# Kernel optimization log

Measured on AMD Instinct MI355X. Metric: run time of the kernel, lower is better.

The kernel has to match this reference:

```python
import jax, jax.numpy as jnp
import numpy as np

D = 128
N_DATA = 100000
N_TASK = 20000
E = 1000000


def _conv_params(key, d):
    ks = jax.random.split(key, 9)
    s = 1.0 / np.sqrt(d)
    return dict(
        Wmn=jax.random.uniform(ks[0], (d, d), jnp.float32, -s, s),
        bmn=jnp.zeros((d,), jnp.float32),
        Wme=jax.random.uniform(ks[1], (d, 1), jnp.float32, -1.0, 1.0),
        bme=jnp.zeros((d,), jnp.float32),
        Wgn=jax.random.uniform(ks[2], (d, d), jnp.float32, -s, s),
        bgn=jnp.zeros((d,), jnp.float32),
        Wge=jax.random.uniform(ks[3], (d, 1), jnp.float32, -1.0, 1.0),
        bge=jnp.zeros((d,), jnp.float32),
        bias=jnp.zeros((d,), jnp.float32),  # HeteConvLayer bias, zeros-init
    )


def setup_inputs() -> dict:
    key = jax.random.key(0)
    ks = jax.random.split(key, 12)
    inp = {
        'x_data': jax.random.normal(ks[0], (N_DATA, D), jnp.float32),
        'x_task': jax.random.normal(ks[1], (N_TASK, D), jnp.float32),
        'src_dt': jax.random.randint(ks[2], (E,), 0, N_DATA, jnp.int32),
        'dst_dt': jax.random.randint(ks[3], (E,), 0, N_TASK, jnp.int32),
        'ef_dt': jax.random.uniform(ks[4], (E, 1), jnp.float32),
        'src_td': jax.random.randint(ks[5], (E,), 0, N_TASK, jnp.int32),
        'dst_td': jax.random.randint(ks[6], (E,), 0, N_DATA, jnp.int32),
        'ef_td': jax.random.uniform(ks[7], (E, 1), jnp.float32),
    }
    # two separate HeteConvLayers (cfg.kg.hete=True)
    for name, k in (('dt', ks[8]), ('td', ks[9])):
        for pn, pv in _conv_params(k, D).items():
            inp[pn + '_' + name] = pv
    s = 1.0 / np.sqrt(D)
    inp['Ws_data'] = jax.random.uniform(ks[10], (D, D), jnp.float32, -s, s)
    inp['bs_data'] = jnp.zeros((D,), jnp.float32)
    inp['Ws_task'] = jax.random.uniform(ks[11], (D, D), jnp.float32, -s, s)
    inp['bs_task'] = jnp.zeros((D,), jnp.float32)
    return inp


def _hete_conv(x_neigh, src, dst, ef, Wmn, bmn, Wme, bme, Wgn, bgn, Wge, bge, bias, n_out):
    xj = x_neigh[src]                                   # [E, D] gather
    msg = xj @ Wmn.T + bmn + ef @ Wme.T + bme           # [E, D]
    gate = jax.nn.sigmoid(xj @ Wgn.T + bgn + ef @ Wge.T + bge) - 0.5  # gate_bias
    msg = msg * gate
    return jax.ops.segment_sum(msg, dst, num_segments=n_out) + bias


def _self_layer(x, Ws, bs):
    return (jax.nn.sigmoid(x @ Ws.T + bs) + 0.5) * x    # SelfLayer, gate_bias=True


def reference(x_data, x_task, src_dt, dst_dt, ef_dt, src_td, dst_td, ef_td,
              Wmn_dt, bmn_dt, Wme_dt, bme_dt, Wgn_dt, bgn_dt, Wge_dt, bge_dt, bias_dt,
              Wmn_td, bmn_td, Wme_td, bme_td, Wgn_td, bgn_td, Wge_td, bge_td, bias_td,
              Ws_data, bs_data, Ws_task, bs_task):
    # message type (data, property, task): neigh=data, self=task
    agg_task = _hete_conv(x_data, src_dt, dst_dt, ef_dt,
                          Wmn_dt, bmn_dt, Wme_dt, bme_dt,
                          Wgn_dt, bgn_dt, Wge_dt, bge_dt, bias_dt, N_TASK)
    # message type (task, property, data): neigh=task, self=data
    agg_data = _hete_conv(x_task, src_td, dst_td, ef_td,
                          Wmn_td, bmn_td, Wme_td, bme_td,
                          Wgn_td, bgn_td, Wge_td, bge_td, bias_td, N_DATA)
    # add self-transform, aggr='add', then Postlayer = ReLU
    data_emb = jax.nn.relu(agg_data + _self_layer(x_data, Ws_data, bs_data))
    task_emb = jax.nn.relu(agg_task + _self_layer(x_task, Ws_task, bs_task))
    # concatenate node-type outputs along node axis for a single output array
    return jnp.concatenate([data_emb, task_emb], axis=0)
```

## Files before the change

### kernel.cpp

```cpp
#include <hip/hip_runtime.h>
#include <hip/hip_bf16.h>
#include <cstdint>
#include <cstddef>

#define D_DIM 128

typedef __attribute__((ext_vector_type(8))) short short8;
typedef __attribute__((ext_vector_type(4))) float f32x4;

__device__ __forceinline__ float sigmoid_fast(float z) {
  return __builtin_amdgcn_rcpf(1.0f + __expf(-z));
}

__device__ __forceinline__ unsigned short f2bf(float f) {
  union { float f; unsigned u; } v; v.f = f;
  unsigned r = v.u + 0x7FFF + ((v.u >> 16) & 1);
  return (unsigned short)(r >> 16);
}
__device__ __forceinline__ float bf_lo(unsigned u) { return __uint_as_float(u << 16); }
__device__ __forceinline__ float bf_hi(unsigned u) { return __uint_as_float(u & 0xFFFF0000u); }

__global__ __launch_bounds__(256) void wconv_kernel(
    const float* __restrict__ s0, const float* __restrict__ s1, const float* __restrict__ s2,
    const float* __restrict__ s3, const float* __restrict__ s4, const float* __restrict__ s5,
    short* __restrict__ dst) {
  int idx = blockIdx.x * 256 + threadIdx.x;
  int mat = idx >> 12;
  int pos = (idx & 4095) * 4;
  const float* s = (mat == 0) ? s0 : (mat == 1) ? s1 : (mat == 2) ? s2
                 : (mat == 3) ? s3 : (mat == 4) ? s4 : s5;
  float4 f = *(const float4*)(s + pos);
  short4 o;
  o.x = (short)f2bf(f.x); o.y = (short)f2bf(f.y);
  o.z = (short)f2bf(f.z); o.w = (short)f2bf(f.w);
  *(short4*)(dst + mat * 16384 + pos) = o;
}

__global__ __launch_bounds__(256) void node_mfma_kernel(
    const float* __restrict__ x,
    const short* __restrict__ Wmnb, const short* __restrict__ Wgnb, const short* __restrict__ Wsb,
    const float* __restrict__ bmn, const float* __restrict__ bme,
    const float* __restrict__ bgn, const float* __restrict__ bge,
    const float* __restrict__ bs, const float* __restrict__ bias_other,
    unsigned int* __restrict__ YG, float* __restrict__ out_init, int n) {
  __shared__ unsigned sh[32][132];
  const int t = threadIdx.x;
  const int wave = t >> 6, lane = t & 63;
  const int q = lane >> 4, l15 = lane & 15;
  const int ng = wave >> 1;
  const int h = (wave & 1) * 64;
  const int base_node = blockIdx.x * 32;
  const int node_base = base_node + ng * 16;

  short8 a[4];
  {
    int m = node_base + l15;
    int mc = m < n ? m : (n - 1);
    const float* xrow = x + (size_t)mc * D_DIM;
#pragma unroll
    for (int ks = 0; ks < 4; ++ks) {
      float4 f0 = *(const float4*)(xrow + ks * 32 + q * 8);
      float4 f1 = *(const float4*)(xrow + ks * 32 + q * 8 + 4);
      union { short8 s; __hip_bfloat162 hh[4]; } u;
      u.hh[0] = __float22bfloat162_rn({f0.x, f0.y});
      u.hh[1] = __float22bfloat162_rn({f0.z, f0.w});
      u.hh[2] = __float22bfloat162_rn({f1.x, f1.y});
      u.hh[3] = __float22bfloat162_rn({f1.z, f1.w});
      a[ks] = u.s;
    }
  }

  f32x4 accY[4], accG[4], accS[4];
#pragma unroll
  for (int nt = 0; nt < 4; ++nt) { accY[nt] = {0,0,0,0}; accG[nt] = {0,0,0,0}; accS[nt] = {0,0,0,0}; }

#pragma unroll
  for (int nt = 0; nt < 4; ++nt) {
    const int row = h + nt * 16 + l15;
#pragma unroll
    for (int ks = 0; ks < 4; ++ks) {
      const int off = row * D_DIM + ks * 32 + q * 8;
      short8 bm  = *(const short8*)(Wmnb + off);
      short8 bg  = *(const short8*)(Wgnb + off);
      short8 bsw = *(const short8*)(Wsb + off);
      accY[nt] = __builtin_amdgcn_mfma_f32_16x16x32_bf16(a[ks], bm,  accY[nt], 0, 0, 0);
      accG[nt] = __builtin_amdgcn_mfma_f32_16x16x32_bf16(a[ks], bg,  accG[nt], 0, 0, 0);
      accS[nt] = __builtin_amdgcn_mfma_f32_16x16x32_bf16(a[ks], bsw, accS[nt], 0, 0, 0);
    }
  }

#pragma unroll
  for (int nt = 0; nt < 4; ++nt) {
    int d = h + nt * 16 + l15;
    float bmv = bmn[d] + bme[d];
    float bgv = bgn[d] + bge[d];
#pragma unroll
    for (int r = 0; r < 4; ++r) {
      union { __hip_bfloat162 hh; unsigned u; } pck;
      pck.hh = __float22bfloat162_rn({accY[nt][r] + bmv, accG[nt][r] + bgv});
      sh[ng * 16 + q * 4 + r][d] = pck.u;
    }
  }
  __syncthreads();
#pragma unroll
  for (int it = 0; it < 4; ++it) {
    int idx = (it * 256 + t) * 4;
    int nl = idx >> 7, dd = idx & 127;
    int node = base_node + nl;
    if (node < n)
      *(uint4*)(YG + (size_t)node * D_DIM + dd) = *(const uint4*)&sh[nl][dd];
  }
  __syncthreads();

  float* shf = (float*)sh;
#pragma unroll
  for (int nt = 0; nt < 4; ++nt) {
    int d = h + nt * 16 + l15;
    float bsv = bs[d];
#pragma unroll
    for (int r = 0; r < 4; ++r)
      shf[(ng * 16 + q * 4 + r) * 132 + d] = sigmoid_fast(accS[nt][r] + bsv) + 0.5f;
  }
  __syncthreads();
#pragma unroll
  for (int it = 0; it < 4; ++it) {
    int idx = (it * 256 + t) * 4;
    int nl = idx >> 7, dd = idx & 127;
    int node = base_node + nl;
    if (node < n) {
      float4 xv = *(const float4*)(x + (size_t)node * D_DIM + dd);
      float4 bo = *(const float4*)(bias_other + dd);
      const float* sp = &shf[nl * 132 + dd];
      float4 o;
      o.x = sp[0] * xv.x + bo.x;
      o.y = sp[1] * xv.y + bo.y;
      o.z = sp[2] * xv.z + bo.z;
      o.w = sp[3] * xv.w + bo.w;
      *(float4*)(out_init + (size_t)node * D_DIM + dd) = o;
    }
  }
}


__global__ __launch_bounds__(256) void hist0_kernel(
    const int* __restrict__ dst_dt, const int* __restrict__ dst_td,
    int* __restrict__ ghist, int nbt, int NB, int E) {
  __shared__ int lh[768];
  int t = threadIdx.x;
  lh[t] = 0; lh[t + 256] = 0; lh[t + 512] = 0;
  __syncthreads();
  for (int i = blockIdx.x * 256 + t; i < E; i += gridDim.x * 256) {
    atomicAdd(&lh[dst_dt[i] >> 6], 1);
    atomicAdd(&lh[nbt + (dst_td[i] >> 8)], 1);
  }
  __syncthreads();
#pragma unroll
  for (int k = 0; k < 3; ++k) {
    int b = t + k * 256;
    int c = lh[b];
    if (b < NB && c) atomicAdd(&ghist[b], c);
  }
}

__global__ __launch_bounds__(256) void bucket_scan_kernel(
    const int* __restrict__ ghist, int* __restrict__ bbase, int* __restrict__ bcur,
    int* __restrict__ offsets, int NB, int n_tot) {
  __shared__ int sc[256];
  int t = threadIdx.x;
  int i0 = t * 3;
  int c0 = (i0     < NB) ? ghist[i0]     : 0;
  int c1 = (i0 + 1 < NB) ? ghist[i0 + 1] : 0;
  int c2 = (i0 + 2 < NB) ? ghist[i0 + 2] : 0;
  int tot = c0 + c1 + c2;
  sc[t] = tot; __syncthreads();
  for (int s = 1; s < 256; s <<= 1) {
    int u = (t >= s) ? sc[t - s] : 0;
    __syncthreads(); sc[t] += u; __syncthreads();
  }
  int base = sc[t] - tot;
  if (i0     < NB) { bbase[i0]     = base;           bcur[i0]     = base; }
  if (i0 + 1 < NB) { bbase[i0 + 1] = base + c0;      bcur[i0 + 1] = base + c0; }
  if (i0 + 2 < NB) { bbase[i0 + 2] = base + c0 + c1; bcur[i0 + 2] = base + c0 + c1; }
  if (t == 255) { bbase[NB] = sc[255]; offsets[n_tot] = sc[255]; }
}

__global__ __launch_bounds__(256) void sort_a_kernel(
    const int* __restrict__ src_dt, const int* __restrict__ dst_dt, const float* __restrict__ ef_dt,
    const int* __restrict__ src_td, const int* __restrict__ dst_td, const float* __restrict__ ef_td,
    int* __restrict__ bcur, int2* __restrict__ eA, int nbt, int NB, int E) {
  __shared__ int lh[768];
  __shared__ int lcur[768];
  int t = threadIdx.x;
  lh[t] = 0; lh[t + 256] = 0; lh[t + 512] = 0;
  __syncthreads();
  int e0 = blockIdx.x * 4096;
  int e1 = min(E, e0 + 4096);
  for (int i = e0 + t; i < e1; i += 256) {
    atomicAdd(&lh[dst_dt[i] >> 6], 1);
    atomicAdd(&lh[nbt + (dst_td[i] >> 8)], 1);
  }
  __syncthreads();
#pragma unroll
  for (int k = 0; k < 3; ++k) {
    int b = t + k * 256;
    int c = lh[b];
    if (b < NB && c) lcur[b] = atomicAdd(&bcur[b], c);
  }
  __syncthreads();
  for (int i = e0 + t; i < e1; i += 256) {
    int c = dst_dt[i];
    int bkt = c >> 6;
    int pos = atomicAdd(&lcur[bkt], 1);
    eA[pos] = make_int2(src_dt[i],
        (int)((__float_as_uint(ef_dt[i]) & 0xFFFFFF00u) | (unsigned)(c & 63)));
    int cd = dst_td[i];
    int bkt2 = nbt + (cd >> 8);
    int pos2 = atomicAdd(&lcur[bkt2], 1);
    eA[pos2] = make_int2(src_td[i],
        (int)((__float_as_uint(ef_td[i]) & 0xFFFFFF00u) | (unsigned)(cd & 255)));
  }
}

__global__ __launch_bounds__(256) void sort_b_kernel(
    const int2* __restrict__ eA, const int* __restrict__ bbase,
    int* __restrict__ offsets, int2* __restrict__ eB,
    int nbt, int n_task, int n_tot) {
  __shared__ int lh[256], sc[256], lcur[256];
  int b = blockIdx.x, t = threadIdx.x;
  int base = bbase[b];
  int cnt = bbase[b + 1] - base;
  int c0, nloc;
  if (b < nbt) { c0 = b << 6; nloc = min(64, n_task - c0); }
  else { c0 = n_task + ((b - nbt) << 8); nloc = min(256, n_tot - c0); }
  lh[t] = 0; __syncthreads();
  for (int i = base + t; i < base + cnt; i += 256)
    atomicAdd(&lh[((unsigned)eA[i].y) & 255u], 1);
  __syncthreads();
  int v = lh[t];
  sc[t] = v; __syncthreads();
  for (int s = 1; s < 256; s <<= 1) {
    int u = (t >= s) ? sc[t - s] : 0;
    __syncthreads(); sc[t] += u; __syncthreads();
  }
  int ex = sc[t] - v;
  lcur[t] = base + ex;
  if (t < nloc) offsets[c0 + t] = base + ex;
  __syncthreads();
  for (int i = base + t; i < base + cnt; i += 256) {
    int2 e = eA[i];
    int pos = atomicAdd(&lcur[((unsigned)e.y) & 255u], 1);
    eB[pos] = e;
  }
}

__device__ __forceinline__ void gstep(float2& acc, int2 e, const unsigned* __restrict__ YG,
                                      int lane, float2 wme, float2 wge) {
  uint2 yg = *(const uint2*)(YG + (size_t)e.x * D_DIM + 2 * lane);
  float f = __int_as_float(e.y & (int)0xFFFFFF00);
  float g0 = sigmoid_fast(fmaf(f, wge.x, bf_hi(yg.x))) - 0.5f;
  float g1 = sigmoid_fast(fmaf(f, wge.y, bf_hi(yg.y))) - 0.5f;
  acc.x += fmaf(f, wme.x, bf_lo(yg.x)) * g0;
  acc.y += fmaf(f, wme.y, bf_lo(yg.y)) * g1;
}

__global__ __launch_bounds__(256) void gather_kernel(
    const unsigned* __restrict__ YG_dt, const unsigned* __restrict__ YG_td,
    const int* __restrict__ offsets, const int2* __restrict__ edata,
    const float* __restrict__ Wme_dt, const float* __restrict__ Wge_dt,
    const float* __restrict__ Wme_td, const float* __restrict__ Wge_td,
    float* __restrict__ out, int n_task, int n_data) {
  int w = (int)((blockIdx.x * 256u + threadIdx.x) >> 6);
  int lane = threadIdx.x & 63;
  if (w >= n_task + n_data) return;
  bool is_dt = w < n_task;
  const unsigned* YG = is_dt ? YG_dt : YG_td;
  const float* Wme = is_dt ? Wme_dt : Wme_td;
  const float* Wge = is_dt ? Wge_dt : Wge_td;
  size_t orow = is_dt ? (size_t)(n_data + w) : (size_t)(w - n_task);
  int beg = __builtin_amdgcn_readfirstlane(offsets[w]);
  int end = __builtin_amdgcn_readfirstlane(offsets[w + 1]);
  float2 wme = *(const float2*)(Wme + 2 * lane);
  float2 wge = *(const float2*)(Wge + 2 * lane);
  float* op = out + orow * D_DIM + 2 * lane;
  float2 acc0 = *(const float2*)op;
  float2 acc1 = {0.0f, 0.0f};
  int p = beg;
  for (; p + 8 <= end; p += 8) {
    int2 e0 = edata[p],     e1 = edata[p + 1], e2 = edata[p + 2], e3 = edata[p + 3];
    int2 e4 = edata[p + 4], e5 = edata[p + 5], e6 = edata[p + 6], e7 = edata[p + 7];
    gstep(acc0, e0, YG, lane, wme, wge);
    gstep(acc1, e1, YG, lane, wme, wge);
    gstep(acc0, e2, YG, lane, wme, wge);
    gstep(acc1, e3, YG, lane, wme, wge);
    gstep(acc0, e4, YG, lane, wme, wge);
    gstep(acc1, e5, YG, lane, wme, wge);
    gstep(acc0, e6, YG, lane, wme, wge);
    gstep(acc1, e7, YG, lane, wme, wge);
  }
  for (; p + 2 <= end; p += 2) {
    int2 e0 = edata[p], e1 = edata[p + 1];
    gstep(acc0, e0, YG, lane, wme, wge);
    gstep(acc1, e1, YG, lane, wme, wge);
  }
  if (p < end) gstep(acc0, edata[p], YG, lane, wme, wge);
  acc0.x = fmaxf(acc0.x + acc1.x, 0.0f);
  acc0.y = fmaxf(acc0.y + acc1.y, 0.0f);
  *(float2*)op = acc0;
}

extern "C" void kernel_launch(void* const* d_in, const int* in_sizes, int n_in,
                              void* d_out, int out_size, void* d_ws, size_t ws_size,
                              hipStream_t stream) {
  const float* x_data  = (const float*)d_in[0];
  const float* x_task  = (const float*)d_in[1];
  const int*   src_dt  = (const int*)d_in[2];
  const int*   dst_dt  = (const int*)d_in[3];
  const float* ef_dt   = (const float*)d_in[4];
  const int*   src_td  = (const int*)d_in[5];
  const int*   dst_td  = (const int*)d_in[6];
  const float* ef_td   = (const float*)d_in[7];
  const float* Wmn_dt  = (const float*)d_in[8];
  const float* bmn_dt  = (const float*)d_in[9];
  const float* Wme_dt  = (const float*)d_in[10];
  const float* bme_dt  = (const float*)d_in[11];
  const float* Wgn_dt  = (const float*)d_in[12];
  const float* bgn_dt  = (const float*)d_in[13];
  const float* Wge_dt  = (const float*)d_in[14];
  const float* bge_dt  = (const float*)d_in[15];
  const float* bias_dt = (const float*)d_in[16];
  const float* Wmn_td  = (const float*)d_in[17];
  const float* bmn_td  = (const float*)d_in[18];
  const float* Wme_td  = (const float*)d_in[19];
  const float* bme_td  = (const float*)d_in[20];
  const float* Wgn_td  = (const float*)d_in[21];
  const float* bgn_td  = (const float*)d_in[22];
  const float* Wge_td  = (const float*)d_in[23];
  const float* bge_td  = (const float*)d_in[24];
  const float* bias_td = (const float*)d_in[25];
  const float* Ws_data = (const float*)d_in[26];
  const float* bs_data = (const float*)d_in[27];
  const float* Ws_task = (const float*)d_in[28];
  const float* bs_task = (const float*)d_in[29];
  float* out = (float*)d_out;

  const int N_DATA = in_sizes[0] / D_DIM;
  const int N_TASK = in_sizes[1] / D_DIM;
  const int E = in_sizes[2];
  const int N_TOT = N_TASK + N_DATA;
  const int NBT = (N_TASK + 63) >> 6;
  const int NBD = (N_DATA + 255) >> 8;
  const int NB = NBT + NBD;

  char* ws = (char*)d_ws;
  size_t off = 0;
  auto alloc = [&](size_t bytes) { void* p = ws + off; off += (bytes + 255) & ~(size_t)255; return p; };
  unsigned int* YG_dt = (unsigned int*)alloc((size_t)N_DATA * D_DIM * 4);
  unsigned int* YG_td = (unsigned int*)alloc((size_t)N_TASK * D_DIM * 4);
  int2* eA     = (int2*)alloc((size_t)2 * E * 8);
  int2* eB     = (int2*)alloc((size_t)2 * E * 8);
  int*  offs   = (int*)alloc((size_t)(N_TOT + 1) * 4);
  int*  ghist  = (int*)alloc(768 * 4);
  int*  bbase  = (int*)alloc(768 * 4);
  int*  bcur   = (int*)alloc(768 * 4);
  short* Wb    = (short*)alloc((size_t)6 * 16384 * 2);
  (void)ws_size; (void)n_in; (void)out_size;

  hipMemsetAsync(ghist, 0, 768 * 4, stream);

  wconv_kernel<<<96, 256, 0, stream>>>(Wmn_dt, Wgn_dt, Ws_data, Wmn_td, Wgn_td, Ws_task, Wb);

  node_mfma_kernel<<<(N_DATA + 31) / 32, 256, 0, stream>>>(
      x_data, Wb, Wb + 16384, Wb + 32768,
      bmn_dt, bme_dt, bgn_dt, bge_dt, bs_data, bias_td,
      YG_dt, out, N_DATA);
  node_mfma_kernel<<<(N_TASK + 31) / 32, 256, 0, stream>>>(
      x_task, Wb + 3 * 16384, Wb + 4 * 16384, Wb + 5 * 16384,
      bmn_td, bme_td, bgn_td, bge_td, bs_task, bias_dt,
      YG_td, out + (size_t)N_DATA * D_DIM, N_TASK);

  hist0_kernel<<<256, 256, 0, stream>>>(dst_dt, dst_td, ghist, NBT, NB, E);
  bucket_scan_kernel<<<1, 256, 0, stream>>>(ghist, bbase, bcur, offs, NB, N_TOT);
  sort_a_kernel<<<(E + 4095) / 4096, 256, 0, stream>>>(
      src_dt, dst_dt, ef_dt, src_td, dst_td, ef_td, bcur, eA, NBT, NB, E);
  sort_b_kernel<<<NB, 256, 0, stream>>>(eA, bbase, offs, eB, NBT, N_TASK, N_TOT);

  gather_kernel<<<(N_TOT + 3) / 4, 256, 0, stream>>>(
      YG_dt, YG_td, offs, eB, Wme_dt, Wge_dt, Wme_td, Wge_td, out, N_TASK, N_DATA);
}
```

Measured before the change: 492.4 us.

## Fuse weight conversion, histogram and scan; merge node GEMM launches; exp2 sigmoid

Result: no change. 492.0 us (-0.1%).

```diff
diff --git a/kernel.cpp b/kernel.cpp
--- a/kernel.cpp
+++ b/kernel.cpp
@@ -4,6 +4,7 @@
 #include <cstddef>
 
 #define D_DIM 128
+#define NEG_LOG2E (-1.44269504f)
 
 typedef __attribute__((ext_vector_type(8))) short short8;
 typedef __attribute__((ext_vector_type(4))) float f32x4;
@@ -20,36 +21,105 @@
 __device__ __forceinline__ float bf_lo(unsigned u) { return __uint_as_float(u << 16); }
 __device__ __forceinline__ float bf_hi(unsigned u) { return __uint_as_float(u & 0xFFFF0000u); }
 
-__global__ __launch_bounds__(256) void wconv_kernel(
+__global__ __launch_bounds__(256) void fused_pre_kernel(
     const float* __restrict__ s0, const float* __restrict__ s1, const float* __restrict__ s2,
     const float* __restrict__ s3, const float* __restrict__ s4, const float* __restrict__ s5,
-    short* __restrict__ dst) {
-  int idx = blockIdx.x * 256 + threadIdx.x;
-  int mat = idx >> 12;
-  int pos = (idx & 4095) * 4;
-  const float* s = (mat == 0) ? s0 : (mat == 1) ? s1 : (mat == 2) ? s2
-                 : (mat == 3) ? s3 : (mat == 4) ? s4 : s5;
-  float4 f = *(const float4*)(s + pos);
-  short4 o;
-  o.x = (short)f2bf(f.x); o.y = (short)f2bf(f.y);
-  o.z = (short)f2bf(f.z); o.w = (short)f2bf(f.w);
-  *(short4*)(dst + mat * 16384 + pos) = o;
-}
-
-__global__ __launch_bounds__(256) void node_mfma_kernel(
-    const float* __restrict__ x,
-    const short* __restrict__ Wmnb, const short* __restrict__ Wgnb, const short* __restrict__ Wsb,
-    const float* __restrict__ bmn, const float* __restrict__ bme,
-    const float* __restrict__ bgn, const float* __restrict__ bge,
-    const float* __restrict__ bs, const float* __restrict__ bias_other,
-    unsigned int* __restrict__ YG, float* __restrict__ out_init, int n) {
+    short* __restrict__ wdst,
+    const int* __restrict__ dst_dt, const int* __restrict__ dst_td,
+    int* __restrict__ ghist, int* __restrict__ done,
+    int* __restrict__ bbase, int* __restrict__ bcur, int* __restrict__ offsets,
+    int nbt, int NB, int E, int n_tot) {
+  __shared__ int lh[768];
+  __shared__ int sc[256];
+  __shared__ int lastflag;
+  int t = threadIdx.x;
+
+  if (blockIdx.x < 96) {
+    int idx = blockIdx.x * 256 + t;
+    int mat = idx >> 12;
+    int pos = (idx & 4095) * 4;
+    const float* s = (mat == 0) ? s0 : (mat == 1) ? s1 : (mat == 2) ? s2
+                   : (mat == 3) ? s3 : (mat == 4) ? s4 : s5;
+    float4 f = *(const float4*)(s + pos);
+    short4 o;
+    o.x = (short)f2bf(f.x); o.y = (short)f2bf(f.y);
+    o.z = (short)f2bf(f.z); o.w = (short)f2bf(f.w);
+    *(short4*)(wdst + mat * 16384 + pos) = o;
+  }
+
+  lh[t] = 0; lh[t + 256] = 0; lh[t + 512] = 0;
+  __syncthreads();
+  for (int i = blockIdx.x * 256 + t; i < E; i += gridDim.x * 256) {
+    atomicAdd(&lh[dst_dt[i] >> 6], 1);
+    atomicAdd(&lh[nbt + (dst_td[i] >> 8)], 1);
+  }
+  __syncthreads();
+#pragma unroll
+  for (int k = 0; k < 3; ++k) {
+    int b = t + k * 256;
+    int c = lh[b];
+    if (b < NB && c) atomicAdd(&ghist[b], c);
+  }
+  __threadfence();
+  __syncthreads();
+  if (t == 0) {
+    int prev = atomicAdd(done, 1);
+    lastflag = (prev == (int)gridDim.x - 1);
+  }
+  __syncthreads();
+  if (!lastflag) return;
+  __threadfence();
+
+  int i0 = t * 3;
+  int c0 = (i0     < NB) ? atomicAdd(&ghist[i0],     0) : 0;
+  int c1 = (i0 + 1 < NB) ? atomicAdd(&ghist[i0 + 1], 0) : 0;
+  int c2 = (i0 + 2 < NB) ? atomicAdd(&ghist[i0 + 2], 0) : 0;
+  int tot = c0 + c1 + c2;
+  sc[t] = tot; __syncthreads();
+  for (int s = 1; s < 256; s <<= 1) {
+    int u = (t >= s) ? sc[t - s] : 0;
+    __syncthreads(); sc[t] += u; __syncthreads();
+  }
+  int base = sc[t] - tot;
+  if (i0     < NB) { bbase[i0]     = base;           bcur[i0]     = base; }
+  if (i0 + 1 < NB) { bbase[i0 + 1] = base + c0;      bcur[i0 + 1] = base + c0; }
+  if (i0 + 2 < NB) { bbase[i0 + 2] = base + c0 + c1; bcur[i0 + 2] = base + c0 + c1; }
+  if (t == 255) { bbase[NB] = sc[255]; offsets[n_tot] = sc[255]; }
+}
+
+__global__ __launch_bounds__(256) void node_mfma_all(
+    const float* __restrict__ x_data, const float* __restrict__ x_task,
+    const short* __restrict__ Wb,
+    const float* __restrict__ bmn_dt, const float* __restrict__ bme_dt,
+    const float* __restrict__ bgn_dt, const float* __restrict__ bge_dt,
+    const float* __restrict__ bmn_td, const float* __restrict__ bme_td,
+    const float* __restrict__ bgn_td, const float* __restrict__ bge_td,
+    const float* __restrict__ bs_data, const float* __restrict__ bs_task,
+    const float* __restrict__ bias_dt, const float* __restrict__ bias_td,
+    unsigned int* __restrict__ YG_dt, unsigned int* __restrict__ YG_td,
+    float* __restrict__ out, int n_data, int n_task, int gd) {
   __shared__ unsigned sh[32][132];
+  const bool is_data = (int)blockIdx.x < gd;
+  const float* x; const short *Wmnb, *Wgnb, *Wsb;
+  const float *bmn, *bme, *bgn, *bge, *bs, *bias_other;
+  unsigned* YG; float* out_init; int n, bid;
+  if (is_data) {
+    x = x_data; Wmnb = Wb; Wgnb = Wb + 16384; Wsb = Wb + 32768;
+    bmn = bmn_dt; bme = bme_dt; bgn = bgn_dt; bge = bge_dt;
+    bs = bs_data; bias_other = bias_td;
+    YG = YG_dt; out_init = out; n = n_data; bid = blockIdx.x;
+  } else {
+    x = x_task; Wmnb = Wb + 3 * 16384; Wgnb = Wb + 4 * 16384; Wsb = Wb + 5 * 16384;
+    bmn = bmn_td; bme = bme_td; bgn = bgn_td; bge = bge_td;
+    bs = bs_task; bias_other = bias_dt;
+    YG = YG_td; out_init = out + (size_t)n_data * D_DIM; n = n_task; bid = blockIdx.x - gd;
+  }
   const int t = threadIdx.x;
   const int wave = t >> 6, lane = t & 63;
   const int q = lane >> 4, l15 = lane & 15;
   const int ng = wave >> 1;
   const int h = (wave & 1) * 64;
-  const int base_node = blockIdx.x * 32;
+  const int base_node = bid * 32;
   const int node_base = base_node + ng * 16;
 
   short8 a[4];
@@ -97,7 +167,8 @@
 #pragma unroll
     for (int r = 0; r < 4; ++r) {
       union { __hip_bfloat162 hh; unsigned u; } pck;
-      pck.hh = __float22bfloat162_rn({accY[nt][r] + bmv, accG[nt][r] + bgv});
+      pck.hh = __float22bfloat162_rn({accY[nt][r] + bmv,
+                                      (accG[nt][r] + bgv) * NEG_LOG2E});
       sh[ng * 16 + q * 4 + r][d] = pck.u;
     }
   }
@@ -141,49 +212,6 @@
   }
 }
 
-
-__global__ __launch_bounds__(256) void hist0_kernel(
-    const int* __restrict__ dst_dt, const int* __restrict__ dst_td,
-    int* __restrict__ ghist, int nbt, int NB, int E) {
-  __shared__ int lh[768];
-  int t = threadIdx.x;
-  lh[t] = 0; lh[t + 256] = 0; lh[t + 512] = 0;
-  __syncthreads();
-  for (int i = blockIdx.x * 256 + t; i < E; i += gridDim.x * 256) {
-    atomicAdd(&lh[dst_dt[i] >> 6], 1);
-    atomicAdd(&lh[nbt + (dst_td[i] >> 8)], 1);
-  }
-  __syncthreads();
-#pragma unroll
-  for (int k = 0; k < 3; ++k) {
-    int b = t + k * 256;
-    int c = lh[b];
-    if (b < NB && c) atomicAdd(&ghist[b], c);
-  }
-}
-
-__global__ __launch_bounds__(256) void bucket_scan_kernel(
-    const int* __restrict__ ghist, int* __restrict__ bbase, int* __restrict__ bcur,
-    int* __restrict__ offsets, int NB, int n_tot) {
-  __shared__ int sc[256];
-  int t = threadIdx.x;
-  int i0 = t * 3;
-  int c0 = (i0     < NB) ? ghist[i0]     : 0;
-  int c1 = (i0 + 1 < NB) ? ghist[i0 + 1] : 0;
-  int c2 = (i0 + 2 < NB) ? ghist[i0 + 2] : 0;
-  int tot = c0 + c1 + c2;
-  sc[t] = tot; __syncthreads();
-  for (int s = 1; s < 256; s <<= 1) {
-    int u = (t >= s) ? sc[t - s] : 0;
-    __syncthreads(); sc[t] += u; __syncthreads();
-  }
-  int base = sc[t] - tot;
-  if (i0     < NB) { bbase[i0]     = base;           bcur[i0]     = base; }
-  if (i0 + 1 < NB) { bbase[i0 + 1] = base + c0;      bcur[i0 + 1] = base + c0; }
-  if (i0 + 2 < NB) { bbase[i0 + 2] = base + c0 + c1; bcur[i0 + 2] = base + c0 + c1; }
-  if (t == 255) { bbase[NB] = sc[255]; offsets[n_tot] = sc[255]; }
-}
-
 __global__ __launch_bounds__(256) void sort_a_kernel(
     const int* __restrict__ src_dt, const int* __restrict__ dst_dt, const float* __restrict__ ef_dt,
     const int* __restrict__ src_td, const int* __restrict__ dst_td, const float* __restrict__ ef_td,
@@ -254,13 +282,13 @@
 }
 
 __device__ __forceinline__ void gstep(float2& acc, int2 e, const unsigned* __restrict__ YG,
-                                      int lane, float2 wme, float2 wge) {
+                                      int lane, float2 wme, float2 wge2) {
   uint2 yg = *(const uint2*)(YG + (size_t)e.x * D_DIM + 2 * lane);
   float f = __int_as_float(e.y & (int)0xFFFFFF00);
-  float g0 = sigmoid_fast(fmaf(f, wge.x, bf_hi(yg.x))) - 0.5f;
-  float g1 = sigmoid_fast(fmaf(f, wge.y, bf_hi(yg.y))) - 0.5f;
-  acc.x += fmaf(f, wme.x, bf_lo(yg.x)) * g0;
-  acc.y += fmaf(f, wme.y, bf_lo(yg.y)) * g1;
+  float g0 = __builtin_amdgcn_rcpf(1.0f + __builtin_amdgcn_exp2f(fmaf(f, wge2.x, bf_hi(yg.x)))) - 0.5f;
+  float g1 = __builtin_amdgcn_rcpf(1.0f + __builtin_amdgcn_exp2f(fmaf(f, wge2.y, bf_hi(yg.y)))) - 0.5f;
+  acc.x = fmaf(fmaf(f, wme.x, bf_lo(yg.x)), g0, acc.x);
+  acc.y = fmaf(fmaf(f, wme.y, bf_lo(yg.y)), g1, acc.y);
 }
 
 __global__ __launch_bounds__(256) void gather_kernel(
@@ -281,6 +309,7 @@
   int end = __builtin_amdgcn_readfirstlane(offsets[w + 1]);
   float2 wme = *(const float2*)(Wme + 2 * lane);
   float2 wge = *(const float2*)(Wge + 2 * lane);
+  float2 wge2 = {wge.x * NEG_LOG2E, wge.y * NEG_LOG2E};
   float* op = out + orow * D_DIM + 2 * lane;
   float2 acc0 = *(const float2*)op;
   float2 acc1 = {0.0f, 0.0f};
@@ -288,21 +317,21 @@
   for (; p + 8 <= end; p += 8) {
     int2 e0 = edata[p],     e1 = edata[p + 1], e2 = edata[p + 2], e3 = edata[p + 3];
     int2 e4 = edata[p + 4], e5 = edata[p + 5], e6 = edata[p + 6], e7 = edata[p + 7];
-    gstep(acc0, e0, YG, lane, wme, wge);
-    gstep(acc1, e1, YG, lane, wme, wge);
-    gstep(acc0, e2, YG, lane, wme, wge);
-    gstep(acc1, e3, YG, lane, wme, wge);
-    gstep(acc0, e4, YG, lane, wme, wge);
-    gstep(acc1, e5, YG, lane, wme, wge);
-    gstep(acc0, e6, YG, lane, wme, wge);
-    gstep(acc1, e7, YG, lane, wme, wge);
+    gstep(acc0, e0, YG, lane, wme, wge2);
+    gstep(acc1, e1, YG, lane, wme, wge2);
+    gstep(acc0, e2, YG, lane, wme, wge2);
+    gstep(acc1, e3, YG, lane, wme, wge2);
+    gstep(acc0, e4, YG, lane, wme, wge2);
+    gstep(acc1, e5, YG, lane, wme, wge2);
+    gstep(acc0, e6, YG, lane, wme, wge2);
+    gstep(acc1, e7, YG, lane, wme, wge2);
   }
   for (; p + 2 <= end; p += 2) {
     int2 e0 = edata[p], e1 = edata[p + 1];
-    gstep(acc0, e0, YG, lane, wme, wge);
-    gstep(acc1, e1, YG, lane, wme, wge);
-  }
-  if (p < end) gstep(acc0, edata[p], YG, lane, wme, wge);
+    gstep(acc0, e0, YG, lane, wme, wge2);
+    gstep(acc1, e1, YG, lane, wme, wge2);
+  }
+  if (p < end) gstep(acc0, edata[p], YG, lane, wme, wge2);
   acc0.x = fmaxf(acc0.x + acc1.x, 0.0f);
   acc0.y = fmaxf(acc0.y + acc1.y, 0.0f);
   *(float2*)op = acc0;
@@ -350,6 +379,8 @@
   const int NBT = (N_TASK + 63) >> 6;
   const int NBD = (N_DATA + 255) >> 8;
   const int NB = NBT + NBD;
+  const int GD = (N_DATA + 31) / 32;
+  const int GT = (N_TASK + 31) / 32;
 
   char* ws = (char*)d_ws;
   size_t off = 0;
@@ -359,27 +390,26 @@
   int2* eA     = (int2*)alloc((size_t)2 * E * 8);
   int2* eB     = (int2*)alloc((size_t)2 * E * 8);
   int*  offs   = (int*)alloc((size_t)(N_TOT + 1) * 4);
-  int*  ghist  = (int*)alloc(768 * 4);
+  int*  ghist  = (int*)alloc(1024 * 4);
   int*  bbase  = (int*)alloc(768 * 4);
   int*  bcur   = (int*)alloc(768 * 4);
   short* Wb    = (short*)alloc((size_t)6 * 16384 * 2);
   (void)ws_size; (void)n_in; (void)out_size;
 
-  hipMemsetAsync(ghist, 0, 768 * 4, stream);
-
-  wconv_kernel<<<96, 256, 0, stream>>>(Wmn_dt, Wgn_dt, Ws_data, Wmn_td, Wgn_td, Ws_task, Wb);
-
-  node_mfma_kernel<<<(N_DATA + 31) / 32, 256, 0, stream>>>(
-      x_data, Wb, Wb + 16384, Wb + 32768,
-      bmn_dt, bme_dt, bgn_dt, bge_dt, bs_data, bias_td,
-      YG_dt, out, N_DATA);
-  node_mfma_kernel<<<(N_TASK + 31) / 32, 256, 0, stream>>>(
-      x_task, Wb + 3 * 16384, Wb + 4 * 16384, Wb + 5 * 16384,
-      bmn_td, bme_td, bgn_td, bge_td, bs_task, bias_dt,
-      YG_td, out + (size_t)N_DATA * D_DIM, N_TASK);
-
-  hist0_kernel<<<256, 256, 0, stream>>>(dst_dt, dst_td, ghist, NBT, NB, E);
-  bucket_scan_kernel<<<1, 256, 0, stream>>>(ghist, bbase, bcur, offs, NB, N_TOT);
+  hipMemsetAsync(ghist, 0, 1024 * 4, stream);
+
+  fused_pre_kernel<<<256, 256, 0, stream>>>(
+      Wmn_dt, Wgn_dt, Ws_data, Wmn_td, Wgn_td, Ws_task, Wb,
+      dst_dt, dst_td, ghist, ghist + 768, bbase, bcur, offs,
+      NBT, NB, E, N_TOT);
+
+  node_mfma_all<<<GD + GT, 256, 0, stream>>>(
+      x_data, x_task, Wb,
+      bmn_dt, bme_dt, bgn_dt, bge_dt,
+      bmn_td, bme_td, bgn_td, bge_td,
+      bs_data, bs_task, bias_dt, bias_td,
+      YG_dt, YG_td, out, N_DATA, N_TASK, GD);
+
   sort_a_kernel<<<(E + 4095) / 4096, 256, 0, stream>>>(
       src_dt, dst_dt, ef_dt, src_td, dst_td, ef_td, bcur, eA, NBT, NB, E);
   sort_b_kernel<<<NB, 256, 0, stream>>>(eA, bbase, offs, eB, NBT, N_TASK, N_TOT);
```
